# Optimization experiments

Measured on AMD Instinct MI355X. Metric: run time of the kernel, lower is better.

Reference implementation:

```python
import jax, jax.numpy as jnp
import numpy as np

HIDDEN = 128
CHNLS = 21
B = 2
T = 15000


def conv1d(x, w, b, stride, pad, groups):
    # x: [N, Cin, L], w: [Cout, Cin/groups, K]
    y = jax.lax.conv_general_dilated(
        x, w, window_strides=(stride,), padding=[(pad, pad)],
        feature_group_count=groups, dimension_numbers=('NCH', 'OIH', 'NCH'))
    return y + b[None, :, None]


def setup_inputs() -> dict:
    key = jax.random.key(0)
    ks = jax.random.split(key, 12)
    d = {}
    d['x'] = jax.random.normal(ks[0], (B, T, CHNLS), dtype=jnp.float32)
    d['ch_vector'] = jax.random.randint(ks[1], (B, CHNLS), 0, CHNLS)
    outs = [HIDDEN // 16 * CHNLS, HIDDEN // 8 * CHNLS, HIDDEN // 4 * CHNLS,
            HIDDEN // 2 * CHNLS, HIDDEN * CHNLS]
    kers = [7, 7, 7, 7, 9]
    for i in range(5):
        d[f'w{i+1}'] = jax.random.normal(ks[2 + i], (outs[i], 1, kers[i]), dtype=jnp.float32) * 0.1
        d[f'b{i+1}'] = jnp.zeros((outs[i],), dtype=jnp.float32)
    d['ch_table'] = jax.random.normal(ks[7], (CHNLS, 512), dtype=jnp.float32) * 0.05
    for i in range(4):
        d[f'mw{i+1}'] = jax.random.normal(ks[8 + i], (1, 1, 4), dtype=jnp.float32) * 0.3
        d[f'mb{i+1}'] = jnp.zeros((1,), dtype=jnp.float32)
    return d


def reference(x, ch_vector, w1, b1, w2, b2, w3, b3, w4, b4, w5, b5,
              ch_table, mw1, mb1, mw2, mb2, mw3, mb3, mw4, mb4):
    # ---- depthwise-style grouped conv stack (groups == in_channels) ----
    h = jnp.transpose(x, (0, 2, 1))                    # [B, CHNLS, T]
    h = conv1d(h, w1, b1, 2, 0, h.shape[1])
    h = conv1d(h, w2, b2, 2, 0, h.shape[1])
    h = conv1d(h, w3, b3, 2, 0, h.shape[1])
    h = conv1d(h, w4, b4, 2, 0, h.shape[1])
    h = conv1d(h, w5, b5, 2, 0, h.shape[1])            # [B, HIDDEN*CHNLS, Tr]

    emb = jnp.transpose(h, (0, 2, 1))                  # [B, Tr, HIDDEN*CHNLS]
    Tr = emb.shape[1]
    emb = emb.reshape(B, Tr, HIDDEN, CHNLS)            # matches torch reshape

    ch_emb = ch_table[ch_vector]                       # [B, CHNLS, 512]
    # torch.einsum('abik, adkj -> abij') with d == 1
    w = jnp.einsum('btik,bkj->btij', emb, ch_emb)      # [B, Tr, HIDDEN, 512]
    w = w.reshape(B, Tr, HIDDEN * 512)

    # ---- per-timestep 1->1 conv stack, batched over B*Tr instead of a loop ----
    z = w.reshape(B * Tr, 1, HIDDEN * 512)
    z = conv1d(z, mw1, mb1, 2, 1, 1)
    z = conv1d(z, mw2, mb2, 2, 1, 1)
    z = jax.nn.gelu(z, approximate=False)
    z = conv1d(z, mw3, mb3, 2, 1, 1)
    z = conv1d(z, mw4, mb4, 2, 1, 1)
    z = jax.nn.gelu(z, approximate=False)              # [B*Tr, 1, HIDDEN*32]
    return z.reshape(B, Tr, HIDDEN * 32)
```

## Files before the change

kernel.cpp:

```cpp
#include <hip/hip_runtime.h>
#include <math.h>


#define NB 2
#define TR 462
#define C5 2688
#define OUTROW 4096

#define T5  21
#define L0T 859
#define L1T 427
#define L2T 211
#define L3T 103
#define L4T 49
#define SS1 432
#define SS2 216
#define SS3 108
#define SS4 49

__device__ __forceinline__ float gelu_exact(float x) {
    return 0.5f * x * (1.0f + erff(x * 0.7071067811865476f));
}

__device__ __forceinline__ int swz(int a) { return a ^ (((a >> 7) & 7) << 2); }

__device__ __forceinline__ void composite10(const float* A, const float* Bv, float* c) {
#pragma unroll
    for (int r = 0; r < 10; ++r) {
        float acc = 0.f;
#pragma unroll
        for (int p = 0; p < 4; ++p) {
            int q = r - 2 * p;
            if (q >= 0 && q < 4) acc = fmaf(A[p], Bv[q], acc);
        }
        c[r] = acc;
    }
}

__global__ __launch_bounds__(256)
void transpose_prep_kernel(const float* __restrict__ in, float* __restrict__ out,
                           const float* __restrict__ table, const int* __restrict__ chv,
                           const float* __restrict__ mw1, const float* __restrict__ mw2,
                           float* __restrict__ cheCT, float* __restrict__ cheLN4)
{
    const int bx = blockIdx.x;
    if (bx >= 118) {
        const int b = bx - 118;
        const int m = threadIdx.x;
        if (m >= 128) return;
        float W1[4], W2[4], c2[10];
#pragma unroll
        for (int q = 0; q < 4; ++q) { W1[q] = mw1[q]; W2[q] = mw2[q]; }
        composite10(W2, W1, c2);
        for (int k = 0; k < 21; ++k) {
            const float* cb = table + (long)chv[b * 21 + k] * 512;
            float acc = 0.f;
            if (m == 0) {
#pragma unroll
                for (int r = 3; r < 10; ++r) acc = fmaf(c2[r], cb[r - 3], acc);
            } else if (m == 127) {
#pragma unroll
                for (int r = 0; r < 7; ++r) acc = fmaf(c2[r], cb[505 + r], acc);
            } else {
                int j0 = 4 * m - 3;
#pragma unroll
                for (int r = 0; r < 10; ++r) acc = fmaf(c2[r], cb[j0 + r], acc);
            }
            cheCT[b * 2688 + m * 21 + k] = acc;
        }
        if (m < 21) {
            const float* cb = table + (long)chv[b * 21 + m] * 512;
            float l = 0.f, n = 0.f;
#pragma unroll
            for (int r = 0; r < 3; ++r)  l = fmaf(c2[r], cb[509 + r], l);
#pragma unroll
            for (int r = 7; r < 10; ++r) n = fmaf(c2[r], cb[r - 7], n);
            cheLN4[b * 84 + m]      = l;
            cheLN4[b * 84 + 21 + m] = n;
            cheLN4[b * 84 + 42 + m] = cb[0];
            cheLN4[b * 84 + 63 + m] = cb[511];
        }
        return;
    }
    __shared__ float s[21 * 257];
    const int b   = bx & 1;
    const int t0  = (bx >> 1) * 256;
    const int tid = threadIdx.x;
    const float* src = in + (long)b * 315000L + (long)t0 * 21L;
    const int limit = 315000 - t0 * 21;
#pragma unroll
    for (int j = 0; j < 21; ++j) {
        int f = tid + j * 256;
        if (f < limit) {
            int t = f / 21, c = f - t * 21;
            s[c * 257 + t] = src[f];
        }
    }
    __syncthreads();
    float* dst = out + (long)b * 315000L + t0;
    if (t0 + tid < 15000) {
#pragma unroll
        for (int c = 0; c < 21; ++c)
            dst[c * 15000 + tid] = s[c * 257 + tid];
    }
}

__global__ __launch_bounds__(256, 5)
void conv_stack_kernel(const float* __restrict__ xT,
                       const float* __restrict__ w1, const float* __restrict__ b1,
                       const float* __restrict__ w2, const float* __restrict__ b2,
                       const float* __restrict__ w3, const float* __restrict__ b3,
                       const float* __restrict__ w4, const float* __restrict__ b4,
                       const float* __restrict__ w5, const float* __restrict__ b5,
                       float* __restrict__ embT)
{
    __shared__ __align__(16) float A[3456];
    __shared__ __align__(16) float B[3456];
    const int tile = blockIdx.x;
    const int c    = blockIdx.y;
    const int b    = blockIdx.z;
    const int tid  = threadIdx.x;
    const int lane = tid & 63;
    const int wq   = tid >> 6;
    const int t0   = tile * T5;

    const float* xp = xT + ((long)b * 21 + c) * 15000L + 32 * t0;
    for (int i = tid; i < L0T; i += 256) A[i] = xp[i];
    __syncthreads();

    auto convK7 = [&](const float* SIN, int sstride, bool from_x,
                      float* SOUT, int ostride,
                      const float* wg, const float* bg, int wbase,
                      int nch, int pairs, int Lout, bool b64st) {
        for (int it = 0; it < (nch >> 2); ++it) {
            const int chg = __builtin_amdgcn_readfirstlane((it << 2) + wq);
            const float* wp = wg + (size_t)(wbase + chg) * 7;
            const float W0 = wp[0], Wa = wp[1], Wb = wp[2], Wc = wp[3],
                        Wd = wp[4], We = wp[5], Wf = wp[6];
            const float bb = bg[wbase + chg];
            const float* sin_ch = SIN + (from_x ? 0 : (chg >> 1) * sstride);
            float* sout_ch = SOUT + chg * ostride;
            for (int j = lane; j < pairs; j += 64) {
                const int p = 2 * j;
                const float* s = sin_ch + p * 2;
                const float4 u0 = *(const float4*)(s);
                const float4 u1 = *(const float4*)(s + 4);
                const float4 u2 = *(const float4*)(s + 8);
                float o0 = bb, o1 = bb;
                o0 = fmaf(W0, u0.x, o0); o0 = fmaf(Wa, u0.y, o0); o0 = fmaf(Wb, u0.z, o0);
                o0 = fmaf(Wc, u0.w, o0); o0 = fmaf(Wd, u1.x, o0); o0 = fmaf(We, u1.y, o0);
                o0 = fmaf(Wf, u1.z, o0);
                o1 = fmaf(W0, u0.z, o1); o1 = fmaf(Wa, u0.w, o1); o1 = fmaf(Wb, u1.x, o1);
                o1 = fmaf(Wc, u1.y, o1); o1 = fmaf(Wd, u1.z, o1); o1 = fmaf(We, u1.w, o1);
                o1 = fmaf(Wf, u2.x, o1);
                if (p + 1 < Lout) {
                    if (b64st) *(float2*)(sout_ch + p) = make_float2(o0, o1);
                    else       { sout_ch[p] = o0; sout_ch[p + 1] = o1; }
                } else {
                    sout_ch[p] = o0;
                }
            }
        }
    };

    convK7(A, 0,   true,  B, SS1, w1, b1, 8 * c,  8,  214, L1T, true);
    __syncthreads();
    convK7(B, SS1, false, A, SS2, w2, b2, 16 * c, 16, 106, L2T, true);
    __syncthreads();
    convK7(A, SS2, false, B, SS3, w3, b3, 32 * c, 32, 52,  L3T, true);
    __syncthreads();
    convK7(B, SS3, false, A, SS4, w4, b4, 64 * c, 64, 25,  L4T, false);
    __syncthreads();

    {
        const int ch5 = tid & 127;
        const int th  = tid >> 7;
        const float* wp = w5 + (size_t)(128 * c + ch5) * 9;
        float V[9];
#pragma unroll
        for (int k = 0; k < 9; ++k) V[k] = wp[k];
        const float bb = b5[128 * c + ch5];
        const float* s4ch = A + (ch5 >> 1) * SS4;
        float* obase = embT + ((long)(b * TR + t0)) * C5 + 128 * c + ch5;
#pragma unroll
        for (int iu = 0; iu < 11; ++iu) {
            const int tl = th + 2 * iu;
            if (tl < T5) {
                const float* sp = s4ch + 2 * tl;
                float acc = bb;
#pragma unroll
                for (int k = 0; k < 9; ++k) acc = fmaf(V[k], sp[k], acc);
                obase[(long)tl * C5] = acc;
            }
        }
    }
}

__global__ __launch_bounds__(512, 4)
void fused_embed_kernel(const float* __restrict__ embT,
                        const float* __restrict__ cheCT,
                        const float* __restrict__ cheLN4,
                        const float* __restrict__ mw1, const float* __restrict__ mb1,
                        const float* __restrict__ mw2, const float* __restrict__ mb2,
                        const float* __restrict__ mw3, const float* __restrict__ mb3,
                        const float* __restrict__ mw4, const float* __restrict__ mb4,
                        float* __restrict__ out)
{
    __shared__ float s_g2[16400];
    __shared__ float s_emb[2688];
    __shared__ float s_ln[84];

    const int t   = blockIdx.x;
    const int b   = blockIdx.y;
    const int tid = threadIdx.x;
    const int i   = tid & 127;
    const int mq  = __builtin_amdgcn_readfirstlane(tid >> 7);

    const float* erow = embT + ((long)(b * TR + t)) * C5;
    for (int j = tid; j < 672; j += 512)
        *(float4*)&s_emb[j * 4] = ((const float4*)erow)[j];
    if (tid < 84) s_ln[tid] = cheLN4[b * 84 + tid];
    if (tid < 4)       s_g2[tid] = 0.f;
    else if (tid < 20) s_g2[16380 + tid] = 0.f;

    float W1[4], W2[4], W3[4], W4[4];
#pragma unroll
    for (int q = 0; q < 4; ++q) { W1[q] = mw1[q]; W2[q] = mw2[q]; W3[q] = mw3[q]; W4[q] = mw4[q]; }
    const float B1 = mb1[0], B2 = mb2[0], B3 = mb3[0], B4 = mb4[0];
    const float Bc = B2 + B1 * (W2[0] + W2[1] + W2[2] + W2[3]);

    __syncthreads();

    float er[21];
#pragma unroll
    for (int k = 0; k < 21; ++k) er[k] = s_emb[i * 21 + k];

    const float* cp = cheCT + (b * 128 + mq * 32) * 21;
#pragma unroll
    for (int mi4 = 0; mi4 < 8; ++mi4) {
        const int m0 = mq * 32 + mi4 * 4;
        const float* cc = cp + mi4 * 84;
        float z0 = Bc, z1 = Bc, z2 = Bc, z3 = Bc;
#pragma unroll
        for (int k = 0; k < 21; ++k) {
            const float e = er[k];
            z0 = fmaf(e, cc[k],      z0);
            z1 = fmaf(e, cc[21 + k], z1);
            z2 = fmaf(e, cc[42 + k], z2);
            z3 = fmaf(e, cc[63 + k], z3);
        }
        if (mi4 == 0 && mq == 0) {
            float corr = 0.f;
            if (i == 0) {
                float w0 = 0.f;
#pragma unroll
                for (int k = 0; k < 21; ++k) w0 = fmaf(er[k], s_ln[42 + k], w0);
                corr = -W2[0] * (B1 + W1[3] * w0);
            } else {
#pragma unroll
                for (int k = 0; k < 21; ++k) corr = fmaf(s_emb[(i - 1) * 21 + k], s_ln[k], corr);
            }
            z0 += corr;
        }
        if (mi4 == 7 && mq == 3) {
            float corr = 0.f;
            if (i == 127) {
                float wl = 0.f;
#pragma unroll
                for (int k = 0; k < 21; ++k) wl = fmaf(er[k], s_ln[63 + k], wl);
                corr = -W2[3] * (B1 + W1[0] * wl);
            } else {
#pragma unroll
                for (int k = 0; k < 21; ++k) corr = fmaf(s_emb[(i + 1) * 21 + k], s_ln[21 + k], corr);
            }
            z3 += corr;
        }
        float4 q;
        q.x = gelu_exact(z0);
        q.y = gelu_exact(z1);
        q.z = gelu_exact(z2);
        q.w = gelu_exact(z3);
        *(float4*)&s_g2[swz(4 + i * 128 + m0)] = q;
    }
    __syncthreads();

    float c4[10];
    composite10(W4, W3, c4);
    const float Bc2 = B4 + B3 * (W4[0] + W4[1] + W4[2] + W4[3]);
    float* orow = out + ((long)(b * TR + t)) * OUTROW;
#pragma unroll
    for (int s = 0; s < 8; ++s) {
        const int p  = tid + 512 * s;
        const int a0 = 4 * p;
        const float4 v0 = *(const float4*)&s_g2[swz(a0)];
        const float4 v1 = *(const float4*)&s_g2[swz(a0 + 4)];
        const float4 v2 = *(const float4*)&s_g2[swz(a0 + 8)];
        const float buf[12] = { v0.x, v0.y, v0.z, v0.w,
                                v1.x, v1.y, v1.z, v1.w,
                                v2.x, v2.y, v2.z, v2.w };
        float z = Bc2;
#pragma unroll
        for (int r = 0; r < 10; ++r) z = fmaf(c4[r], buf[r + 1], z);
        if (p == 0)    z -= W4[0] * (B3 + W3[3] * s_g2[swz(4)]);
        if (p == 4095) z -= W4[3] * (B3 + W3[0] * s_g2[swz(16387)]);
        orow[p] = gelu_exact(z);
    }
}

extern "C" void kernel_launch(void* const* d_in, const int* in_sizes, int n_in,
                              void* d_out, int out_size, void* d_ws, size_t ws_size,
                              hipStream_t stream)
{
    const float* x   = (const float*)d_in[0];
    const int*   chv = (const int*)d_in[1];
    const float* w1  = (const float*)d_in[2];  const float* b1 = (const float*)d_in[3];
    const float* w2  = (const float*)d_in[4];  const float* b2 = (const float*)d_in[5];
    const float* w3  = (const float*)d_in[6];  const float* b3 = (const float*)d_in[7];
    const float* w4  = (const float*)d_in[8];  const float* b4 = (const float*)d_in[9];
    const float* w5  = (const float*)d_in[10]; const float* b5 = (const float*)d_in[11];
    const float* tab = (const float*)d_in[12];
    const float* mw1 = (const float*)d_in[13]; const float* mb1 = (const float*)d_in[14];
    const float* mw2 = (const float*)d_in[15]; const float* mb2 = (const float*)d_in[16];
    const float* mw3 = (const float*)d_in[17]; const float* mb3 = (const float*)d_in[18];
    const float* mw4 = (const float*)d_in[19]; const float* mb4 = (const float*)d_in[20];
    float* outp = (float*)d_out;

    float* ws     = (float*)d_ws;
    float* xT     = ws;
    float* embT   = ws + 630000;
    float* cheCT  = ws + 3113712;
    float* cheLN4 = ws + 3119088;

    transpose_prep_kernel<<<120, 256, 0, stream>>>(x, xT, tab, chv, mw1, mw2,
                                                   cheCT, cheLN4);
    {
        dim3 grid(22, 21, NB);
        conv_stack_kernel<<<grid, 256, 0, stream>>>(xT, w1, b1, w2, b2, w3, b3,
                                                    w4, b4, w5, b5, embT);
    }
    {
        dim3 grid(TR, NB);
        fused_embed_kernel<<<grid, 512, 0, stream>>>(embT, cheCT, cheLN4,
                                                     mw1, mb1, mw2, mb2, mw3, mb3, mw4, mb4,
                                                     outp);
    }
}
```

Baseline: 60.56 us.

## Fuse transpose and prep into conv stack with strided loads and larger time tiles

Removes the separate transpose kernel: the conv stack now reads x directly with a stride of 21 channels, and the channel-embedding prep work runs in an extra tile column of the same launch. Time tiles double from 21 to 42 output steps, so the grid shrinks from 22x21x2 to 12x21x2 blocks, halving the redundant halo loads. This saves one launch and the xT round trip through global memory. In exchange the input loads are uncoalesced, there is less parallelism, and shared memory per block grows to about 48KB, which lowers occupancy.

```diff
diff --git a/kernel.cpp b/kernel.cpp
--- a/kernel.cpp
+++ b/kernel.cpp
@@ -7,16 +7,16 @@
 #define C5 2688
 #define OUTROW 4096
 
-#define T5  21
-#define L0T 859
-#define L1T 427
-#define L2T 211
-#define L3T 103
-#define L4T 49
-#define SS1 432
-#define SS2 216
-#define SS3 108
-#define SS4 49
+#define T5  42
+#define L0T 1531
+#define L1T 763
+#define L2T 379
+#define L3T 187
+#define L4T 91
+#define SS1 768
+#define SS2 384
+#define SS3 192
+#define SS4 93
 
 __device__ __forceinline__ float gelu_exact(float x) {
     return 0.5f * x * (1.0f + erff(x * 0.7071067811865476f));
@@ -38,16 +38,25 @@
 }
 
 __global__ __launch_bounds__(256)
-void transpose_prep_kernel(const float* __restrict__ in, float* __restrict__ out,
-                           const float* __restrict__ table, const int* __restrict__ chv,
-                           const float* __restrict__ mw1, const float* __restrict__ mw2,
-                           float* __restrict__ cheCT, float* __restrict__ cheLN4)
+void conv_stack_prep_kernel(const float* __restrict__ x,
+                            const float* __restrict__ w1, const float* __restrict__ b1,
+                            const float* __restrict__ w2, const float* __restrict__ b2,
+                            const float* __restrict__ w3, const float* __restrict__ b3,
+                            const float* __restrict__ w4, const float* __restrict__ b4,
+                            const float* __restrict__ w5, const float* __restrict__ b5,
+                            const float* __restrict__ table, const int* __restrict__ chv,
+                            const float* __restrict__ mw1, const float* __restrict__ mw2,
+                            float* __restrict__ embT,
+                            float* __restrict__ cheCT, float* __restrict__ cheLN4)
 {
-    const int bx = blockIdx.x;
-    if (bx >= 118) {
-        const int b = bx - 118;
-        const int m = threadIdx.x;
-        if (m >= 128) return;
+    const int tile = blockIdx.x;
+    const int c    = blockIdx.y;
+    const int b    = blockIdx.z;
+    const int tid  = threadIdx.x;
+
+    if (tile == 11) {
+        if (c != 0 || tid >= 128) return;
+        const int m = tid;
         float W1[4], W2[4], c2[10];
 #pragma unroll
         for (int q = 0; q < 4; ++q) { W1[q] = mw1[q]; W2[q] = mw2[q]; }
@@ -82,50 +91,17 @@
         }
         return;
     }
-    __shared__ float s[21 * 257];
-    const int b   = bx & 1;
-    const int t0  = (bx >> 1) * 256;
-    const int tid = threadIdx.x;
-    const float* src = in + (long)b * 315000L + (long)t0 * 21L;
-    const int limit = 315000 - t0 * 21;
-#pragma unroll
-    for (int j = 0; j < 21; ++j) {
-        int f = tid + j * 256;
-        if (f < limit) {
-            int t = f / 21, c = f - t * 21;
-            s[c * 257 + t] = src[f];
-        }
-    }
-    __syncthreads();
-    float* dst = out + (long)b * 315000L + t0;
-    if (t0 + tid < 15000) {
-#pragma unroll
-        for (int c = 0; c < 21; ++c)
-            dst[c * 15000 + tid] = s[c * 257 + tid];
-    }
-}
-
-__global__ __launch_bounds__(256, 5)
-void conv_stack_kernel(const float* __restrict__ xT,
-                       const float* __restrict__ w1, const float* __restrict__ b1,
-                       const float* __restrict__ w2, const float* __restrict__ b2,
-                       const float* __restrict__ w3, const float* __restrict__ b3,
-                       const float* __restrict__ w4, const float* __restrict__ b4,
-                       const float* __restrict__ w5, const float* __restrict__ b5,
-                       float* __restrict__ embT)
-{
-    __shared__ __align__(16) float A[3456];
-    __shared__ __align__(16) float B[3456];
-    const int tile = blockIdx.x;
-    const int c    = blockIdx.y;
-    const int b    = blockIdx.z;
-    const int tid  = threadIdx.x;
+
+    __shared__ __align__(16) float A[6144];
+    __shared__ __align__(16) float B[6144];
     const int lane = tid & 63;
     const int wq   = tid >> 6;
     const int t0   = tile * T5;
 
-    const float* xp = xT + ((long)b * 21 + c) * 15000L + 32 * t0;
-    for (int i = tid; i < L0T; i += 256) A[i] = xp[i];
+    {
+        const float* xp = x + (long)b * 315000L + (long)(32 * t0) * 21L + c;
+        for (int i = tid; i < L0T; i += 256) A[i] = xp[(long)i * 21L];
+    }
     __syncthreads();
 
     auto convK7 = [&](const float* SIN, int sstride, bool from_x,
@@ -163,13 +139,13 @@
         }
     };
 
-    convK7(A, 0,   true,  B, SS1, w1, b1, 8 * c,  8,  214, L1T, true);
-    __syncthreads();
-    convK7(B, SS1, false, A, SS2, w2, b2, 16 * c, 16, 106, L2T, true);
-    __syncthreads();
-    convK7(A, SS2, false, B, SS3, w3, b3, 32 * c, 32, 52,  L3T, true);
-    __syncthreads();
-    convK7(B, SS3, false, A, SS4, w4, b4, 64 * c, 64, 25,  L4T, false);
+    convK7(A, 0,   true,  B, SS1, w1, b1, 8 * c,  8,  382, L1T, true);
+    __syncthreads();
+    convK7(B, SS1, false, A, SS2, w2, b2, 16 * c, 16, 190, L2T, true);
+    __syncthreads();
+    convK7(A, SS2, false, B, SS3, w3, b3, 32 * c, 32, 94,  L3T, true);
+    __syncthreads();
+    convK7(B, SS3, false, A, SS4, w4, b4, 64 * c, 64, 46,  L4T, false);
     __syncthreads();
 
     {
@@ -183,15 +159,13 @@
         const float* s4ch = A + (ch5 >> 1) * SS4;
         float* obase = embT + ((long)(b * TR + t0)) * C5 + 128 * c + ch5;
 #pragma unroll
-        for (int iu = 0; iu < 11; ++iu) {
+        for (int iu = 0; iu < 21; ++iu) {
             const int tl = th + 2 * iu;
-            if (tl < T5) {
-                const float* sp = s4ch + 2 * tl;
-                float acc = bb;
-#pragma unroll
-                for (int k = 0; k < 9; ++k) acc = fmaf(V[k], sp[k], acc);
-                obase[(long)tl * C5] = acc;
-            }
+            const float* sp = s4ch + 2 * tl;
+            float acc = bb;
+#pragma unroll
+            for (int k = 0; k < 9; ++k) acc = fmaf(V[k], sp[k], acc);
+            obase[(long)tl * C5] = acc;
         }
     }
 }
@@ -326,17 +300,16 @@
     float* outp = (float*)d_out;
 
     float* ws     = (float*)d_ws;
-    float* xT     = ws;
-    float* embT   = ws + 630000;
-    float* cheCT  = ws + 3113712;
-    float* cheLN4 = ws + 3119088;
-
-    transpose_prep_kernel<<<120, 256, 0, stream>>>(x, xT, tab, chv, mw1, mw2,
-                                                   cheCT, cheLN4);
+    float* embT   = ws;
+    float* cheCT  = ws + 2483712;
+    float* cheLN4 = ws + 2489088;
+
     {
-        dim3 grid(22, 21, NB);
-        conv_stack_kernel<<<grid, 256, 0, stream>>>(xT, w1, b1, w2, b2, w3, b3,
-                                                    w4, b4, w5, b5, embT);
+        dim3 grid(12, 21, NB);
+        conv_stack_prep_kernel<<<grid, 256, 0, stream>>>(x, w1, b1, w2, b2, w3, b3,
+                                                         w4, b4, w5, b5,
+                                                         tab, chv, mw1, mw2,
+                                                         embT, cheCT, cheLN4);
     }
     {
         dim3 grid(TR, NB);
```

After: 51.22 us. 1.18x faster.
